# Performance work log

Hardware: AMD Instinct MI355X
Metric: run time of the kernel (lower is better)

## Reference

```python
import jax, jax.numpy as jnp
import numpy as np

NUM_TIMESTEPS = 8  # num_timesteps default of CSSMDeiT3Block
LN_EPS = 1e-6      # flax nn.LayerNorm default


def _layernorm(x, scale, bias):
    mu = jnp.mean(x, axis=-1, keepdims=True)
    var = jnp.mean(jnp.square(x - mu), axis=-1, keepdims=True)
    return (x - mu) * jax.lax.rsqrt(var + LN_EPS) * scale + bias


def setup_inputs() -> dict:
    key = jax.random.key(0)
    ks = jax.random.split(key, 8)
    B, H, W, C = 32, 14, 14, 768
    HID = 4 * C
    s = lambda fan: np.float32(1.0 / np.sqrt(fan))
    return {
        "x": jax.random.normal(ks[0], (B, H, W, C), jnp.float32),
        # norm1
        "ln1_scale": jnp.ones((C,), jnp.float32),
        "ln1_bias": jnp.zeros((C,), jnp.float32),
        # GatedCSSM (opponent, concat_xy=True, sigmoid gate)
        "W_in": jax.random.normal(ks[1], (C, C), jnp.float32) * s(C),
        "b_in": jnp.zeros((C,), jnp.float32),
        "W_gate": jax.random.normal(ks[2], (2 * C, C), jnp.float32) * s(2 * C),
        "b_gate": jnp.zeros((C,), jnp.float32),
        "a_decay": jax.random.uniform(ks[3], (C,), jnp.float32, 0.5, 0.99),
        "b_rot": jax.random.normal(ks[4], (C,), jnp.float32) * 0.1,
        "W_out": jax.random.normal(ks[5], (C, C), jnp.float32) * s(C),
        "b_out": jnp.zeros((C,), jnp.float32),
        # layer scales (init_values = 1e-6)
        "gamma1": jnp.full((C,), 1e-6, jnp.float32),
        # norm2 + MLP
        "ln2_scale": jnp.ones((C,), jnp.float32),
        "ln2_bias": jnp.zeros((C,), jnp.float32),
        "W1": jax.random.normal(ks[6], (C, HID), jnp.float32) * s(C),
        "b1": jnp.zeros((HID,), jnp.float32),
        "W2": jax.random.normal(ks[7], (HID, C), jnp.float32) * s(HID),
        "b2": jnp.zeros((C,), jnp.float32),
        "gamma2": jnp.full((C,), 1e-6, jnp.float32),
    }


def reference(x, ln1_scale, ln1_bias, W_in, b_in, W_gate, b_gate, a_decay,
              b_rot, W_out, b_out, gamma1, ln2_scale, ln2_bias,
              W1, b1, W2, b2, gamma2):
    # ---- branch 1: pre-norm -> GatedCSSM (temporal recurrence) -> layerscale -> residual
    residual = x
    xn = _layernorm(x, ln1_scale, ln1_bias)
    # input is repeated over T timesteps, so project once and reuse
    u = xn @ W_in + b_in                       # (B,H,W,C)
    z0 = jnp.zeros_like(u)

    def step(carry, _):
        hx, hy = carry
        # concat_xy=True: gate computed from both opponent states
        g = jax.nn.sigmoid(jnp.concatenate([hx, hy], axis=-1) @ W_gate + b_gate)
        # opponent (rotation/decay) state-space update, gated
        hx_n = g * (a_decay * hx - b_rot * hy) + u
        hy_n = g * (b_rot * hx + a_decay * hy)
        return (hx_n, hy_n), None

    (hx, _hy), _ = jax.lax.scan(step, (z0, z0), None, length=NUM_TIMESTEPS)
    y = hx @ W_out + b_out                     # last-timestep readout (B,H,W,C)
    x = residual + y * gamma1                  # DropPath is identity (rate 0, deterministic)

    # ---- branch 2: pre-norm -> MLP(gelu) -> layerscale -> residual
    residual = x
    xn = _layernorm(x, ln2_scale, ln2_bias)
    h = jax.nn.gelu(xn @ W1 + b1)
    m = h @ W2 + b2
    return residual + m * gamma2
```

## Files before the change

kernel.cpp:

```cpp
#include <hip/hip_runtime.h>
#include <math.h>

typedef __bf16 bf16x8 __attribute__((ext_vector_type(8)));
typedef float  f32x4  __attribute__((ext_vector_type(4)));

#define NROWS 6272
#define CDIM  768
#define HIDD  3072

#define EPI_UINIT 0
#define EPI_GELU  2
#define EPI_RES   3

__device__ __forceinline__ void gload16(const void* g, void* l) {
    __builtin_amdgcn_global_load_lds(
        (const __attribute__((address_space(1))) void*)(uintptr_t)g,
        (__attribute__((address_space(3))) void*)(uintptr_t)l,
        16, 0, 0);
}

__device__ __forceinline__ void xcd_swz(int& m, int& n) {
    const int gx = gridDim.x;
    const int nwg = gx * gridDim.y;
    const int orig = blockIdx.x + gx * blockIdx.y;
    const int q = nwg >> 3, r = nwg & 7;
    const int xcd = orig & 7, loc = orig >> 3;
    const int wg = (xcd < r ? xcd * (q + 1) : r * (q + 1) + (xcd - r) * q) + loc;
    m = wg / gx;
    n = wg % gx;
}

template <int BM, int BN>
__device__ __forceinline__ void gemm_core(const __bf16* __restrict__ A, int lda,
                                          const __bf16* __restrict__ BT, int K,
                                          int m0, int n0,
                                          __bf16* As, __bf16* Bs,
                                          f32x4 acc[BM / 32][BN / 32]) {
    constexpr int RF = BM / 32;
    constexpr int CF = BN / 32;
    constexpr int ASZ = BM * 32;
    constexpr int BSZ = BN * 32;
    const int t  = threadIdx.x;
    const int w  = t >> 6;
    const int l  = t & 63;
    const int wm = w >> 1, wn = w & 1;
    const int rsub = t >> 2;
    const int ke   = (t & 3) * 8;
    const int fr = l & 15;
    const int kq = (l >> 4) * 8;

    const __bf16* gA = A  + (size_t)(m0 + rsub) * lda + ke;
    const __bf16* gB = BT + (size_t)(n0 + rsub) * K   + ke;

    #pragma unroll
    for (int h = 0; h < BM / 64; ++h)
        gload16(gA + (size_t)(h * 64) * lda, As + w * 512 + h * 2048);
    #pragma unroll
    for (int h = 0; h < BN / 64; ++h)
        gload16(gB + (size_t)(h * 64) * K, Bs + w * 512 + h * 2048);

    const int NT = K >> 5;
    #pragma unroll 2
    for (int kt = 0; kt < NT; ++kt) {
        const int cur = kt & 1;
        __syncthreads();
        if (kt + 1 < NT) {
            const int k0 = (kt + 1) * 32;
            const int nb = cur ^ 1;
            #pragma unroll
            for (int h = 0; h < BM / 64; ++h)
                gload16(gA + (size_t)(h * 64) * lda + k0, As + nb * ASZ + w * 512 + h * 2048);
            #pragma unroll
            for (int h = 0; h < BN / 64; ++h)
                gload16(gB + (size_t)(h * 64) * K + k0, Bs + nb * BSZ + w * 512 + h * 2048);
        }
        const __bf16* cA = As + cur * ASZ;
        const __bf16* cB = Bs + cur * BSZ;
        bf16x8 av[RF], bv[CF];
        #pragma unroll
        for (int i = 0; i < RF; ++i)
            av[i] = *(const bf16x8*)&cA[(wm * (BM / 2) + i * 16 + fr) * 32 + kq];
        #pragma unroll
        for (int j = 0; j < CF; ++j)
            bv[j] = *(const bf16x8*)&cB[(wn * (BN / 2) + j * 16 + fr) * 32 + kq];
        #pragma unroll
        for (int i = 0; i < RF; ++i)
            #pragma unroll
            for (int j = 0; j < CF; ++j)
                acc[i][j] = __builtin_amdgcn_mfma_f32_16x16x32_bf16(av[i], bv[j], acc[i][j], 0, 0, 0);
    }
}

__global__ __launch_bounds__(256) void transpose_all(const float* __restrict__ W_in,
                                                     const float* __restrict__ W_gate,
                                                     const float* __restrict__ W_out,
                                                     const float* __restrict__ W1,
                                                     const float* __restrict__ W2,
                                                     __bf16* __restrict__ WT_in,
                                                     __bf16* __restrict__ WT_gate,
                                                     __bf16* __restrict__ WT_out,
                                                     __bf16* __restrict__ WT1,
                                                     __bf16* __restrict__ WT2) {
    const int bid = blockIdx.x;
    const float* W; __bf16* WT; int K, N, gx, local;
    if (bid < 576)        { W = W_in;   WT = WT_in;   K = 768;  N = 768;  gx = 24; local = bid; }
    else if (bid < 1728)  { W = W_gate; WT = WT_gate; K = 1536; N = 768;  gx = 24; local = bid - 576; }
    else if (bid < 2304)  { W = W_out;  WT = WT_out;  K = 768;  N = 768;  gx = 24; local = bid - 1728; }
    else if (bid < 4608)  { W = W1;     WT = WT1;     K = 768;  N = 3072; gx = 96; local = bid - 2304; }
    else                  { W = W2;     WT = WT2;     K = 3072; N = 768;  gx = 24; local = bid - 4608; }
    const int nb = (local % gx) * 32;
    const int kb = (local / gx) * 32;

    __shared__ float tile[32][33];
    const int tx = threadIdx.x, ty = threadIdx.y;
    #pragma unroll
    for (int r = 0; r < 4; ++r)
        tile[ty + r * 8][tx] = W[(size_t)(kb + ty + r * 8) * N + nb + tx];
    __syncthreads();
    #pragma unroll
    for (int r = 0; r < 4; ++r)
        WT[(size_t)(nb + ty + r * 8) * K + kb + tx] = (__bf16)tile[tx][ty + r * 8];
}

__global__ __launch_bounds__(256) void ln_kernel(const float* __restrict__ x,
                                                 const float* __restrict__ sc,
                                                 const float* __restrict__ bi,
                                                 __bf16* __restrict__ o) {
    const int row = blockIdx.x;
    const float* xr = x + (size_t)row * CDIM;
    __bf16* orow = o + (size_t)row * CDIM;
    const int t = threadIdx.x;

    float v0 = xr[t], v1 = xr[t + 256], v2 = xr[t + 512];
    float s = v0 + v1 + v2;

    __shared__ float sm[8];
    #pragma unroll
    for (int off = 32; off > 0; off >>= 1) s += __shfl_xor(s, off);
    const int wid = t >> 6, lane = t & 63;
    if (lane == 0) sm[wid] = s;
    __syncthreads();
    const float mu = (sm[0] + sm[1] + sm[2] + sm[3]) * (1.0f / 768.0f);

    const float d0 = v0 - mu, d1 = v1 - mu, d2 = v2 - mu;
    float s2 = d0 * d0 + d1 * d1 + d2 * d2;
    #pragma unroll
    for (int off = 32; off > 0; off >>= 1) s2 += __shfl_xor(s2, off);
    if (lane == 0) sm[4 + wid] = s2;
    __syncthreads();
    const float var = (sm[4] + sm[5] + sm[6] + sm[7]) * (1.0f / 768.0f);
    const float r = rsqrtf(var + 1e-6f);

    orow[t]       = (__bf16)(d0 * r * sc[t]       + bi[t]);
    orow[t + 256] = (__bf16)(d1 * r * sc[t + 256] + bi[t + 256]);
    orow[t + 512] = (__bf16)(d2 * r * sc[t + 512] + bi[t + 512]);
}

template <int EPI, int BM, int BN>
__global__ __launch_bounds__(256) void mm_bf16(const __bf16* __restrict__ A, int lda,
                                               const __bf16* __restrict__ BT,
                                               const float* __restrict__ bias,
                                               const float* __restrict__ gamma,
                                               const float* __restrict__ res, int ldr,
                                               void* __restrict__ outv, int ldo,
                                               int K, __bf16* __restrict__ hxy0) {
    constexpr int RF = BM / 32;
    constexpr int CF = BN / 32;
    __shared__ __bf16 As[2 * BM * 32];
    __shared__ __bf16 Bs[2 * BN * 32];
    int mb, nb;
    xcd_swz(mb, nb);
    const int m0 = mb * BM, n0 = nb * BN;

    f32x4 acc[RF][CF];
    #pragma unroll
    for (int i = 0; i < RF; ++i)
        #pragma unroll
        for (int j = 0; j < CF; ++j)
            acc[i][j] = f32x4{0.f, 0.f, 0.f, 0.f};

    gemm_core<BM, BN>(A, lda, BT, K, m0, n0, As, Bs, acc);

    const int l = threadIdx.x & 63;
    const int w = threadIdx.x >> 6;
    const int wm = w >> 1, wn = w & 1;
    const int fr = l & 15;
    const int row0 = m0 + wm * (BM / 2);
    const int col0 = n0 + wn * (BN / 2);
    #pragma unroll
    for (int i = 0; i < RF; ++i) {
        #pragma unroll
        for (int j = 0; j < CF; ++j) {
            const int col = col0 + j * 16 + fr;
            const float bsv = bias[col];
            #pragma unroll
            for (int r = 0; r < 4; ++r) {
                const int row = row0 + i * 16 + (l >> 4) * 4 + r;
                float z = acc[i][j][r] + bsv;
                if (EPI == EPI_UINIT) {
                    ((__bf16*)outv)[(size_t)row * ldo + col] = (__bf16)z;
                    hxy0[(size_t)row * 1536 + col] = (__bf16)z;
                    hxy0[(size_t)row * 1536 + 768 + col] = (__bf16)0.f;
                } else if (EPI == EPI_GELU) {
                    const float v = 1.5957691216f * z * (1.0f + 0.044715f * z * z);
                    const float sg = 1.0f / (1.0f + __expf(-v));
                    ((__bf16*)outv)[(size_t)row * ldo + col] = (__bf16)(z * sg);
                } else {
                    const float zz = res[(size_t)row * ldr + col] + z * gamma[col];
                    ((float*)outv)[(size_t)row * ldo + col] = zz;
                }
            }
        }
    }
}

template <bool LAST>
__global__ __launch_bounds__(256) void gate_step(const __bf16* __restrict__ hxy_cur,
                                                 const __bf16* __restrict__ WT_gate,
                                                 const float* __restrict__ b_gate,
                                                 const __bf16* __restrict__ u,
                                                 const float* __restrict__ ad,
                                                 const float* __restrict__ br,
                                                 __bf16* __restrict__ hxy_next) {
    constexpr int BM = 64, BN = 64;
    __shared__ __bf16 As[2 * BM * 32];
    __shared__ __bf16 Bs[2 * BN * 32];
    int mb, nb;
    xcd_swz(mb, nb);
    const int m0 = mb * BM, n0 = nb * BN;

    f32x4 acc[2][2];
    #pragma unroll
    for (int i = 0; i < 2; ++i)
        #pragma unroll
        for (int j = 0; j < 2; ++j)
            acc[i][j] = f32x4{0.f, 0.f, 0.f, 0.f};

    gemm_core<BM, BN>(hxy_cur, 1536, WT_gate, 1536, m0, n0, As, Bs, acc);

    const int l = threadIdx.x & 63;
    const int w = threadIdx.x >> 6;
    const int wm = w >> 1, wn = w & 1;
    const int fr = l & 15;
    const int row0 = m0 + wm * 32;
    const int col0 = n0 + wn * 32;
    #pragma unroll
    for (int i = 0; i < 2; ++i) {
        #pragma unroll
        for (int j = 0; j < 2; ++j) {
            const int col = col0 + j * 16 + fr;
            const float bg = b_gate[col];
            const float av = ad[col];
            const float bv = br[col];
            #pragma unroll
            for (int r = 0; r < 4; ++r) {
                const int row = row0 + i * 16 + (l >> 4) * 4 + r;
                float z = acc[i][j][r] + bg;
                z = 1.0f / (1.0f + __expf(-z));
                const size_t base = (size_t)row * 1536 + col;
                const float hx = (float)hxy_cur[base];
                const float hy = (float)hxy_cur[base + 768];
                const float uf = (float)u[(size_t)row * 768 + col];
                hxy_next[base] = (__bf16)(z * (av * hx - bv * hy) + uf);
                if (!LAST)
                    hxy_next[base + 768] = (__bf16)(z * (bv * hx + av * hy));
            }
        }
    }
}

extern "C" void kernel_launch(void* const* d_in, const int* in_sizes, int n_in,
                              void* d_out, int out_size, void* d_ws, size_t ws_size,
                              hipStream_t stream) {
    (void)in_sizes; (void)n_in; (void)out_size;
    const float* x      = (const float*)d_in[0];
    const float* ln1_s  = (const float*)d_in[1];
    const float* ln1_b  = (const float*)d_in[2];
    const float* W_in   = (const float*)d_in[3];
    const float* b_in   = (const float*)d_in[4];
    const float* W_gate = (const float*)d_in[5];
    const float* b_gate = (const float*)d_in[6];
    const float* a_dec  = (const float*)d_in[7];
    const float* b_rot  = (const float*)d_in[8];
    const float* W_out  = (const float*)d_in[9];
    const float* b_out  = (const float*)d_in[10];
    const float* gamma1 = (const float*)d_in[11];
    const float* ln2_s  = (const float*)d_in[12];
    const float* ln2_b  = (const float*)d_in[13];
    const float* W1     = (const float*)d_in[14];
    const float* b1     = (const float*)d_in[15];
    const float* W2     = (const float*)d_in[16];
    const float* b2     = (const float*)d_in[17];
    const float* gamma2 = (const float*)d_in[18];
    float* out = (float*)d_out;

    if (ws_size < 92000000) return;
    char* w8 = (char*)d_ws;
    __bf16* WT_in   = (__bf16*)(w8);
    __bf16* WT_gate = (__bf16*)(w8 + 1179648);
    __bf16* WT_out  = (__bf16*)(w8 + 3538944);
    __bf16* WT1     = (__bf16*)(w8 + 4718592);
    __bf16* WT2     = (__bf16*)(w8 + 9437184);
    float*  x1      = (float*)(w8 + 14155776);
    __bf16* xn      = (__bf16*)(w8 + 33423360);
    __bf16* u       = (__bf16*)(w8 + 43057152);
    __bf16* hxy_a   = (__bf16*)(w8 + 52690944);
    __bf16* hxy_b   = (__bf16*)(w8 + 71958528);
    __bf16* h       = (__bf16*)(w8 + 52690944);

    transpose_all<<<6912, dim3(32, 8), 0, stream>>>(W_in, W_gate, W_out, W1, W2,
                                                    WT_in, WT_gate, WT_out, WT1, WT2);

    const dim3 gC(12, 98);
    const dim3 gH(24, 49);

    ln_kernel<<<NROWS, 256, 0, stream>>>(x, ln1_s, ln1_b, xn);
    mm_bf16<EPI_UINIT, 64, 64><<<gC, 256, 0, stream>>>(xn, 768, WT_in, b_in,
                                                       nullptr, nullptr, 0, u, 768, 768, hxy_a);
    __bf16* cur = hxy_a;
    __bf16* nxt = hxy_b;
    for (int ts = 1; ts < 8; ++ts) {
        if (ts == 7)
            gate_step<true><<<gC, 256, 0, stream>>>(cur, WT_gate, b_gate, u, a_dec, b_rot, nxt);
        else
            gate_step<false><<<gC, 256, 0, stream>>>(cur, WT_gate, b_gate, u, a_dec, b_rot, nxt);
        __bf16* tmp = cur; cur = nxt; nxt = tmp;
    }
    mm_bf16<EPI_RES, 64, 64><<<gC, 256, 0, stream>>>(cur, 1536, WT_out, b_out,
                                                     gamma1, x, 768, x1, 768, 768, nullptr);
    ln_kernel<<<NROWS, 256, 0, stream>>>(x1, ln2_s, ln2_b, xn);
    mm_bf16<EPI_GELU, 128, 128><<<gH, 256, 0, stream>>>(xn, 768, WT1, b1,
                                                        nullptr, nullptr, 0, h, 3072, 768, nullptr);
    mm_bf16<EPI_RES, 64, 64><<<gC, 256, 0, stream>>>(h, 3072, WT2, b2,
                                                     gamma2, x1, 768, out, 768, 3072, nullptr);
}
```

Before: 569.4 us.

## Replace double-buffered GEMM main loop with 4-stage LDS pipeline using vmcnt waits

The shared GEMM core now keeps three K-tiles of async global-to-LDS loads in flight across four LDS buffers instead of one. It waits with explicit s_waitcnt vmcnt counts and raw s_barrier rather than a full __syncthreads each iteration. The aim is to hide global memory latency behind MFMA work in all matmul and gate-step kernels. LDS use per block doubles, which may lower occupancy. The manually unrolled schedule assumes the K-tile count is a multiple of four and that no other vector-memory ops are outstanding.

```diff
diff --git a/kernel.cpp b/kernel.cpp
--- a/kernel.cpp
+++ b/kernel.cpp
@@ -17,6 +17,15 @@
         (const __attribute__((address_space(1))) void*)(uintptr_t)g,
         (__attribute__((address_space(3))) void*)(uintptr_t)l,
         16, 0, 0);
+}
+
+template <int N>
+__device__ __forceinline__ void waitcnt_vm() {
+    if constexpr (N == 0)      asm volatile("s_waitcnt vmcnt(0)" ::: "memory");
+    else if constexpr (N == 2) asm volatile("s_waitcnt vmcnt(2)" ::: "memory");
+    else if constexpr (N == 4) asm volatile("s_waitcnt vmcnt(4)" ::: "memory");
+    else if constexpr (N == 8) asm volatile("s_waitcnt vmcnt(8)" ::: "memory");
+    __builtin_amdgcn_sched_barrier(0);
 }
 
 __device__ __forceinline__ void xcd_swz(int& m, int& n) {
@@ -36,10 +45,11 @@
                                           int m0, int n0,
                                           __bf16* As, __bf16* Bs,
                                           f32x4 acc[BM / 32][BN / 32]) {
-    constexpr int RF = BM / 32;
-    constexpr int CF = BN / 32;
+    constexpr int RF  = BM / 32;
+    constexpr int CF  = BN / 32;
     constexpr int ASZ = BM * 32;
     constexpr int BSZ = BN * 32;
+    constexpr int LPT = BM / 64 + BN / 64;
     const int t  = threadIdx.x;
     const int w  = t >> 6;
     const int l  = t & 63;
@@ -52,30 +62,18 @@
     const __bf16* gA = A  + (size_t)(m0 + rsub) * lda + ke;
     const __bf16* gB = BT + (size_t)(n0 + rsub) * K   + ke;
 
-    #pragma unroll
-    for (int h = 0; h < BM / 64; ++h)
-        gload16(gA + (size_t)(h * 64) * lda, As + w * 512 + h * 2048);
-    #pragma unroll
-    for (int h = 0; h < BN / 64; ++h)
-        gload16(gB + (size_t)(h * 64) * K, Bs + w * 512 + h * 2048);
-
-    const int NT = K >> 5;
-    #pragma unroll 2
-    for (int kt = 0; kt < NT; ++kt) {
-        const int cur = kt & 1;
-        __syncthreads();
-        if (kt + 1 < NT) {
-            const int k0 = (kt + 1) * 32;
-            const int nb = cur ^ 1;
-            #pragma unroll
-            for (int h = 0; h < BM / 64; ++h)
-                gload16(gA + (size_t)(h * 64) * lda + k0, As + nb * ASZ + w * 512 + h * 2048);
-            #pragma unroll
-            for (int h = 0; h < BN / 64; ++h)
-                gload16(gB + (size_t)(h * 64) * K + k0, Bs + nb * BSZ + w * 512 + h * 2048);
-        }
-        const __bf16* cA = As + cur * ASZ;
-        const __bf16* cB = Bs + cur * BSZ;
+    auto STAGE = [&](int kt, int buf) {
+        const int k0 = kt * 32;
+        #pragma unroll
+        for (int h = 0; h < BM / 64; ++h)
+            gload16(gA + (size_t)(h * 64) * lda + k0, As + buf * ASZ + w * 512 + h * 2048);
+        #pragma unroll
+        for (int h = 0; h < BN / 64; ++h)
+            gload16(gB + (size_t)(h * 64) * K + k0, Bs + buf * BSZ + w * 512 + h * 2048);
+    };
+    auto COMPUTE = [&](int buf) {
+        const __bf16* cA = As + buf * ASZ;
+        const __bf16* cB = Bs + buf * BSZ;
         bf16x8 av[RF], bv[CF];
         #pragma unroll
         for (int i = 0; i < RF; ++i)
@@ -88,7 +86,29 @@
             #pragma unroll
             for (int j = 0; j < CF; ++j)
                 acc[i][j] = __builtin_amdgcn_mfma_f32_16x16x32_bf16(av[i], bv[j], acc[i][j], 0, 0, 0);
+    };
+
+    STAGE(0, 0); STAGE(1, 1); STAGE(2, 2);
+    const int NT = K >> 5;
+
+    for (int kt = 0; kt + 4 < NT; kt += 4) {
+        waitcnt_vm<2 * LPT>(); __builtin_amdgcn_s_barrier();
+        STAGE(kt + 3, 3); COMPUTE(0);
+        waitcnt_vm<2 * LPT>(); __builtin_amdgcn_s_barrier();
+        STAGE(kt + 4, 0); COMPUTE(1);
+        waitcnt_vm<2 * LPT>(); __builtin_amdgcn_s_barrier();
+        STAGE(kt + 5, 1); COMPUTE(2);
+        waitcnt_vm<2 * LPT>(); __builtin_amdgcn_s_barrier();
+        STAGE(kt + 6, 2); COMPUTE(3);
     }
+    waitcnt_vm<2 * LPT>(); __builtin_amdgcn_s_barrier();
+    STAGE(NT - 1, 3); COMPUTE(0);
+    waitcnt_vm<2 * LPT>(); __builtin_amdgcn_s_barrier();
+    COMPUTE(1);
+    waitcnt_vm<LPT>();     __builtin_amdgcn_s_barrier();
+    COMPUTE(2);
+    waitcnt_vm<0>();       __builtin_amdgcn_s_barrier();
+    COMPUTE(3);
 }
 
 __global__ __launch_bounds__(256) void transpose_all(const float* __restrict__ W_in,
@@ -166,8 +186,8 @@
                                                int K, __bf16* __restrict__ hxy0) {
     constexpr int RF = BM / 32;
     constexpr int CF = BN / 32;
-    __shared__ __bf16 As[2 * BM * 32];
-    __shared__ __bf16 Bs[2 * BN * 32];
+    __shared__ __bf16 As[4 * BM * 32];
+    __shared__ __bf16 Bs[4 * BN * 32];
     int mb, nb;
     xcd_swz(mb, nb);
     const int m0 = mb * BM, n0 = nb * BN;
@@ -223,8 +243,8 @@
                                                  const float* __restrict__ br,
                                                  __bf16* __restrict__ hxy_next) {
     constexpr int BM = 64, BN = 64;
-    __shared__ __bf16 As[2 * BM * 32];
-    __shared__ __bf16 Bs[2 * BN * 32];
+    __shared__ __bf16 As[4 * BM * 32];
+    __shared__ __bf16 Bs[4 * BN * 32];
     int mb, nb;
     xcd_swz(mb, nb);
     const int m0 = mb * BM, n0 = nb * BN;
```

Result: faster. 552.0 us (-3.1%).
